# Kernel optimization log

Measured on AMD Instinct MI355X. Metric: run time of the kernel, lower is better.

Reference implementation:

```python
import jax, jax.numpy as jnp
import numpy as np

EMBED_DIM = 1024
NUM_HEADS = 16
HEAD_DIM = EMBED_DIM // NUM_HEADS


def setup_inputs() -> dict:
    key = jax.random.key(0)
    ks = jax.random.split(key, 10)
    s = 1.0 / np.sqrt(EMBED_DIM)
    inp = {
        "x1": jax.random.normal(ks[0], (4, 1024, EMBED_DIM), jnp.float32),
        "x2": jax.random.normal(ks[1], (4, 2048, EMBED_DIM), jnp.float32),
        "Wq": jax.random.normal(ks[2], (EMBED_DIM, EMBED_DIM), jnp.float32) * s,
        "bq": jnp.zeros((EMBED_DIM,), jnp.float32),
        "Wk": jax.random.normal(ks[3], (EMBED_DIM, EMBED_DIM), jnp.float32) * s,
        "bk": jnp.zeros((EMBED_DIM,), jnp.float32),
        "Wv": jax.random.normal(ks[4], (EMBED_DIM, EMBED_DIM), jnp.float32) * s,
        "bv": jnp.zeros((EMBED_DIM,), jnp.float32),
        "Wo": jax.random.normal(ks[5], (EMBED_DIM, EMBED_DIM), jnp.float32) * s,
        "bo": jnp.zeros((EMBED_DIM,), jnp.float32),
    }
    return inp


def reference(x1, x2, Wq, bq, Wk, bk, Wv, bv, Wo, bo):
    B, Sq, E = x1.shape
    Skv = x2.shape[1]
    H, D = NUM_HEADS, HEAD_DIM
    # linear projections (PyTorch Linear: x @ W.T + b)
    q = (x1 @ Wq.T + bq).reshape(B, Sq, H, D).transpose(0, 2, 1, 3)   # [B,H,Sq,D]
    k = (x2 @ Wk.T + bk).reshape(B, Skv, H, D).transpose(0, 2, 1, 3)  # [B,H,Skv,D]
    v = (x2 @ Wv.T + bv).reshape(B, Skv, H, D).transpose(0, 2, 1, 3)
    scores = jnp.einsum("bhqd,bhkd->bhqk", q, k) / jnp.sqrt(jnp.float32(D))
    attn = jax.nn.softmax(scores, axis=-1)
    out = jnp.einsum("bhqk,bhkd->bhqd", attn, v)
    out = out.transpose(0, 2, 1, 3).reshape(B, Sq, E)
    return out @ Wo.T + bo
```

## Files before the change

kernel.cpp:

```cpp
#include <hip/hip_runtime.h>

typedef __attribute__((ext_vector_type(8))) short short8;
typedef __attribute__((ext_vector_type(4))) short short4v;
typedef __attribute__((ext_vector_type(4))) float f32x4;
typedef _Float16 half8 __attribute__((ext_vector_type(8)));

#define ASYNC16(g, l) __builtin_amdgcn_global_load_lds( \
    (__attribute__((address_space(1))) void*)(g), \
    (__attribute__((address_space(3))) void*)(l), 16, 0, 0)

__device__ __forceinline__ short f2bf(float f) {
  union { float f; unsigned u; } v; v.f = f;
  unsigned r = v.u + 0x7fffu + ((v.u >> 16) & 1u);
  return (short)(r >> 16);
}

__device__ __forceinline__ short f2h(float f) {
  _Float16 h = (_Float16)f;
  return __builtin_bit_cast(short, h);
}

__device__ __forceinline__ unsigned pkh2(float a, float b) {
  return __builtin_bit_cast(unsigned, __builtin_amdgcn_cvt_pkrtz(a, b));
}

__device__ __forceinline__ f32x4 fzero4() {
  f32x4 z; z[0] = 0.f; z[1] = 0.f; z[2] = 0.f; z[3] = 0.f; return z;
}

__device__ __forceinline__ void wg_barrier() {
  asm volatile("s_waitcnt lgkmcnt(0)\n\ts_barrier" ::: "memory");
}

__device__ __forceinline__ void wait4_barrier() {
  asm volatile("s_waitcnt vmcnt(4)\n\ts_barrier" ::: "memory");
}
__device__ __forceinline__ void wait6_barrier() {
  asm volatile("s_waitcnt vmcnt(6)\n\ts_barrier" ::: "memory");
}
__device__ __forceinline__ void wait0_barrier() {
  asm volatile("s_waitcnt vmcnt(0)\n\ts_barrier" ::: "memory");
}

__global__ __launch_bounds__(256) void cvt_all(
    const float* __restrict__ x1, const float* __restrict__ x2,
    const float* __restrict__ wq, const float* __restrict__ wk,
    const float* __restrict__ wv, const float* __restrict__ wo,
    short* __restrict__ dst) {
  long e = ((long)blockIdx.x * 256 + threadIdx.x) * 4;
  const float* src; long loc;
  if (e < 4194304L)       { src = x1; loc = e; }
  else if (e < 12582912L) { src = x2; loc = e - 4194304L; }
  else if (e < 13631488L) { src = wq; loc = e - 12582912L; }
  else if (e < 14680064L) { src = wk; loc = e - 13631488L; }
  else if (e < 15728640L) { src = wv; loc = e - 14680064L; }
  else                    { src = wo; loc = e - 15728640L; }
  float4 v = *(const float4*)(src + loc);
  short4v o;
  o[0] = f2bf(v.x); o[1] = f2bf(v.y); o[2] = f2bf(v.z); o[3] = f2bf(v.w);
  *(short4v*)(dst + e) = o;
}

__global__ __launch_bounds__(256) void proj(
    const short* __restrict__ xb1, const short* __restrict__ xb2,
    const short* __restrict__ wqp, const short* __restrict__ wkp, const short* __restrict__ wvp,
    const float* __restrict__ bq, const float* __restrict__ bk, const float* __restrict__ bv,
    short* __restrict__ qb, short* __restrict__ kb, short* __restrict__ vb) {
  __shared__ short smem[16384];
  const int tid = threadIdx.x, w = tid >> 6, lane = tid & 63;
  const int quad = lane >> 4, col = lane & 15;
  const int waveM = (w >> 1) * 64, waveN = (w & 1) * 64;
  const int my = blockIdx.x, bn = blockIdx.y * 128;
  const short* A; const short* W; const float* bias; int mode, bm;
  if (my < 32)      { A = xb1; W = wqp; bias = bq; mode = 0; bm = my * 128; }
  else if (my < 96) { A = xb2; W = wkp; bias = bk; mode = 1; bm = (my - 32) * 128; }
  else              { A = xb2; W = wvp; bias = bv; mode = 2; bm = (my - 96) * 128; }

  f32x4 acc[4][4];
  for (int mi = 0; mi < 4; ++mi)
    for (int ni = 0; ni < 4; ++ni)
      acc[mi][ni] = fzero4();

  const int srow = w * 16 + (lane >> 2), scol = (lane & 3) * 8;
  const short* ga = A + (size_t)(bm + srow) * 1024 + scol;
  const short* gb = W + (size_t)(bn + srow) * 1024 + scol;

  auto stage = [&](int b, int kk) {
    short* lA = smem + b * 8192 + w * 512;
    short* lB = smem + b * 8192 + 4096 + w * 512;
    ASYNC16(ga + kk,         lA);
    ASYNC16(ga + kk + 65536, lA + 2048);
    ASYNC16(gb + kk,         lB);
    ASYNC16(gb + kk + 65536, lB + 2048);
  };
  auto compute = [&](int b) {
    const short* As_ = smem + b * 8192;
    const short* Bs_ = As_ + 4096;
    short8 af[4], bf[4];
    for (int mi = 0; mi < 4; ++mi)
      af[mi] = *(const short8*)(As_ + (waveM + mi * 16 + col) * 32 + quad * 8);
    for (int ni = 0; ni < 4; ++ni)
      bf[ni] = *(const short8*)(Bs_ + (waveN + ni * 16 + col) * 32 + quad * 8);
    for (int mi = 0; mi < 4; ++mi)
      for (int ni = 0; ni < 4; ++ni)
        acc[mi][ni] = __builtin_amdgcn_mfma_f32_16x16x32_bf16(af[mi], bf[ni], acc[mi][ni], 0, 0, 0);
  };

  stage(0, 0);
  stage(1, 32);
  for (int it = 0; it < 30; ++it) {
    wait4_barrier();
    compute(it & 1);
    wg_barrier();
    stage(it & 1, (it + 2) * 32);
  }
  wait4_barrier();
  compute(0);
  wait0_barrier();
  compute(1);

  for (int ni = 0; ni < 4; ++ni) {
    int nn = waveN + ni * 16 + col;
    float bvl = bias[bn + nn];
    for (int mi = 0; mi < 4; ++mi) {
      int m0 = waveM + mi * 16 + quad * 4;
      for (int r = 0; r < 4; ++r) {
        int m = m0 + r;
        float val = acc[mi][ni][r] + bvl;
        short sv;
        if (mode == 0)      sv = f2bf(val * 0.18033688011112042f);
        else if (mode == 1) sv = f2bf(val);
        else                sv = f2h(val);
        smem[m * 128 + (nn ^ ((m & 15) << 3))] = sv;
      }
    }
  }
  __syncthreads();
  if (mode < 2) {
    const int S = (mode == 0) ? 1024 : 2048;
    short* outp = (mode == 0) ? qb : kb;
    const int bb = bm / S, s0 = bm & (S - 1), h0 = bn >> 6;
    for (int it = 0; it < 8; ++it) {
      int f = (it * 256 + tid) * 8;
      int hh = f >> 13, rem = f & 8191, m = rem >> 6, d = rem & 63;
      int nn = hh * 64 + d;
      short8 val = *(const short8*)&smem[m * 128 + (nn ^ ((m & 15) << 3))];
      *(short8*)(outp + ((((size_t)(bb * 16 + h0 + hh)) * S + s0 + m) * 64 + d)) = val;
    }
  } else {
    const int bb = bm >> 11, s0 = bm & 2047, kt0 = s0 >> 6, h0 = bn >> 6;
    for (int it = 0; it < 8; ++it) {
      int f = (it * 256 + tid) * 8;
      int hh = f >> 13, rem = f & 8191, ktl = rem >> 12, r3 = rem & 4095;
      int d = r3 >> 6, kvp0 = r3 & 63;
      int nn = hh * 64 + d;
      short8 val;
      for (int j = 0; j < 8; ++j) {
        int kvp = kvp0 + j;
        int kv = ((kvp & 3) << 4) | (kvp >> 2);
        int m = ktl * 64 + kv;
        val[j] = smem[m * 128 + (nn ^ ((m & 15) << 3))];
      }
      *(short8*)(vb + ((((size_t)(bb * 16 + h0 + hh)) * 32 + (kt0 + ktl)) * 4096) + d * 64 + kvp0) = val;
    }
  }
}

__global__ __launch_bounds__(256) void out_gemm(
    const short* __restrict__ A, const short* __restrict__ W,
    const float* __restrict__ bias, float* __restrict__ out) {
  __shared__ short smem[24576];
  const int tid = threadIdx.x, w = tid >> 6, lane = tid & 63;
  const int quad = lane >> 4, col = lane & 15;
  const int waveM = (w >> 1) * 64, waveN = (w & 1) * 32;
  const int bn = blockIdx.x * 64, bm = blockIdx.y * 128;

  f32x4 acc[4][2];
  for (int mi = 0; mi < 4; ++mi)
    for (int ni = 0; ni < 2; ++ni)
      acc[mi][ni] = fzero4();

  const int arow = w * 16 + (lane >> 2), ac = (lane & 3) * 8;
  const short* ga = A + (size_t)(bm + arow) * 1024 + ac;
  const short* gb = W + (size_t)(bn + (tid >> 2)) * 1024 + (tid & 3) * 8;

  auto stage = [&](int b, int kk) {
    short* base = smem + b * 12288;
    short* lA0 = base + w * 512;
    short* lA1 = base + 4096 + w * 512;
    short* lB0 = base + 8192 + w * 512;
    short* lB1 = base + 10240 + w * 512;
    ASYNC16(ga + kk,              lA0);
    ASYNC16(ga + kk + 65536,      lA0 + 2048);
    ASYNC16(ga + kk + 32,         lA1);
    ASYNC16(ga + kk + 32 + 65536, lA1 + 2048);
    ASYNC16(gb + kk,              lB0);
    ASYNC16(gb + kk + 32,         lB1);
  };
  auto compute = [&](int b) {
    const short* base = smem + b * 12288;
    for (int kh = 0; kh < 2; ++kh) {
      const short* Ash = base + kh * 4096;
      const short* Bsh = base + 8192 + kh * 2048;
      short8 af[4], bf[2];
      for (int mi = 0; mi < 4; ++mi)
        af[mi] = *(const short8*)(Ash + (waveM + mi * 16 + col) * 32 + quad * 8);
      for (int ni = 0; ni < 2; ++ni)
        bf[ni] = *(const short8*)(Bsh + (waveN + ni * 16 + col) * 32 + quad * 8);
      for (int mi = 0; mi < 4; ++mi)
        for (int ni = 0; ni < 2; ++ni)
          acc[mi][ni] = __builtin_amdgcn_mfma_f32_16x16x32_bf16(af[mi], bf[ni], acc[mi][ni], 0, 0, 0);
    }
  };

  stage(0, 0);
  stage(1, 64);
  for (int it = 0; it < 14; ++it) {
    wait6_barrier();
    compute(it & 1);
    wg_barrier();
    stage(it & 1, (it + 2) * 64);
  }
  wait6_barrier();
  compute(0);
  wait0_barrier();
  compute(1);

  for (int ni = 0; ni < 2; ++ni) {
    int n = bn + waveN + ni * 16 + col;
    float bvl = bias[n];
    for (int mi = 0; mi < 4; ++mi) {
      int m0 = bm + waveM + mi * 16 + quad * 4;
      for (int r = 0; r < 4; ++r)
        out[(size_t)(m0 + r) * 1024 + n] = acc[mi][ni][r] + bvl;
    }
  }
}

__global__ __launch_bounds__(256, 2) void attn(
    const short* __restrict__ Q, const short* __restrict__ K,
    const short* __restrict__ V, short* __restrict__ O) {
  __shared__ short Ks[128 * 72];
  __shared__ short Vs[80 * 136];
  __shared__ short Ps[128 * 136];
  const int tid = threadIdx.x, w = tid >> 6, lane = tid & 63;
  const int quad = lane >> 4, col = lane & 15;
  const int bh = blockIdx.x, qt = blockIdx.y;
  const int b = bh >> 4, h = bh & 15;
  const int qbase = w * 32;

  const short* qp = Q + ((size_t)bh * 1024 + qt * 128) * 64;
  const short* kp = K + (size_t)bh * 131072;
  const short* vp = V + (size_t)bh * 131072;

  short8 aq[2][2];
  for (int mi = 0; mi < 2; ++mi) {
    const short* qr = qp + (qbase + mi * 16 + col) * 64 + quad * 8;
    aq[mi][0] = *(const short8*)qr;
    aq[mi][1] = *(const short8*)(qr + 32);
  }

  f32x4 oa[2][5];
  for (int mi = 0; mi < 2; ++mi)
    for (int ni = 0; ni < 5; ++ni)
      oa[mi][ni] = fzero4();

  for (int i = tid; i < 16 * 136; i += 256)
    Vs[64 * 136 + i] = (i < 136) ? (short)0x3C00 : (short)0;

  const int krow = lane + (w >> 1) * 64, kch = (w & 1) * 32;
  const int vd = lane, vch = w & 1, vkh = (w >> 1) * 32;

  short8 kpre[4], vpre[4];
  {
    const short* kg = kp + krow * 64 + kch;
    const short* vg = vp + vch * 4096 + vd * 64 + vkh;
    for (int i = 0; i < 4; ++i) kpre[i] = *(const short8*)(kg + i * 8);
    for (int i = 0; i < 4; ++i) vpre[i] = *(const short8*)(vg + i * 8);
  }

  for (int kt = 0; kt < 16; ++kt) {
    wg_barrier();
    for (int i = 0; i < 4; ++i)
      *(short8*)&Ks[krow * 72 + kch + i * 8] = kpre[i];
    for (int i = 0; i < 4; ++i)
      *(short8*)&Vs[vd * 136 + vch * 64 + vkh + i * 8] = vpre[i];
    {
      int ktn = (kt < 15) ? kt + 1 : kt;
      const short* kg = kp + ktn * 8192 + krow * 64 + kch;
      const short* vg = vp + (2 * ktn + vch) * 4096 + vd * 64 + vkh;
      for (int i = 0; i < 4; ++i) kpre[i] = *(const short8*)(kg + i * 8);
      for (int i = 0; i < 4; ++i) vpre[i] = *(const short8*)(vg + i * 8);
    }
    wg_barrier();

    f32x4 sf[2][8];
    for (int nk = 0; nk < 8; ++nk) {
      short8 bk0 = *(const short8*)&Ks[(nk * 16 + col) * 72 + quad * 8];
      short8 bk1 = *(const short8*)&Ks[(nk * 16 + col) * 72 + 32 + quad * 8];
      f32x4 z0 = fzero4(), z1 = fzero4();
      z0 = __builtin_amdgcn_mfma_f32_16x16x32_bf16(aq[0][0], bk0, z0, 0, 0, 0);
      z0 = __builtin_amdgcn_mfma_f32_16x16x32_bf16(aq[0][1], bk1, z0, 0, 0, 0);
      z1 = __builtin_amdgcn_mfma_f32_16x16x32_bf16(aq[1][0], bk0, z1, 0, 0, 0);
      z1 = __builtin_amdgcn_mfma_f32_16x16x32_bf16(aq[1][1], bk1, z1, 0, 0, 0);
      sf[0][nk] = z0;
      sf[1][nk] = z1;
    }

    for (int mi = 0; mi < 2; ++mi)
      for (int nk = 0; nk < 8; ++nk)
        for (int r = 0; r < 4; ++r)
          sf[mi][nk][r] = __builtin_amdgcn_exp2f(sf[mi][nk][r]);
    for (int mi = 0; mi < 2; ++mi)
      for (int r = 0; r < 4; ++r) {
        int row = qbase + mi * 16 + quad * 4 + r;
        uint2 d0, d1;
        d0.x = pkh2(sf[mi][0][r], sf[mi][1][r]);
        d0.y = pkh2(sf[mi][2][r], sf[mi][3][r]);
        d1.x = pkh2(sf[mi][4][r], sf[mi][5][r]);
        d1.y = pkh2(sf[mi][6][r], sf[mi][7][r]);
        *(uint2*)&Ps[row * 136 + col * 4]      = d0;
        *(uint2*)&Ps[row * 136 + 64 + col * 4] = d1;
      }

    for (int ks = 0; ks < 4; ++ks) {
      int koff = ks * 32 + quad * 8;
      half8 ap0 = *(const half8*)&Ps[(qbase + col) * 136 + koff];
      half8 ap1 = *(const half8*)&Ps[(qbase + 16 + col) * 136 + koff];
      for (int ni = 0; ni < 5; ++ni) {
        half8 bv = *(const half8*)&Vs[(ni * 16 + col) * 136 + koff];
        oa[0][ni] = __builtin_amdgcn_mfma_f32_16x16x32_f16(ap0, bv, oa[0][ni], 0, 0, 0);
        oa[1][ni] = __builtin_amdgcn_mfma_f32_16x16x32_f16(ap1, bv, oa[1][ni], 0, 0, 0);
      }
    }
  }

  float inv[2][4];
  for (int mi = 0; mi < 2; ++mi)
    for (int r = 0; r < 4; ++r) {
      float s = __shfl(oa[mi][4][r], lane & 48);
      inv[mi][r] = 1.f / s;
    }
  __syncthreads();
  for (int mi = 0; mi < 2; ++mi)
    for (int ni = 0; ni < 4; ++ni)
      for (int r = 0; r < 4; ++r)
        Ps[(qbase + mi * 16 + quad * 4 + r) * 64 + ni * 16 + col] = f2bf(oa[mi][ni][r] * inv[mi][r]);
  __syncthreads();
  for (int it = 0; it < 4; ++it) {
    int f = (it * 256 + tid) * 8;
    int q = f >> 6, d = f & 63;
    short8 val = *(const short8*)&Ps[q * 64 + d];
    *(short8*)(O + ((size_t)(b * 1024 + qt * 128 + q)) * 1024 + h * 64 + d) = val;
  }
}

extern "C" void kernel_launch(void* const* d_in, const int* in_sizes, int n_in,
                              void* d_out, int out_size, void* d_ws, size_t ws_size,
                              hipStream_t stream) {
  const float* x1 = (const float*)d_in[0];
  const float* x2 = (const float*)d_in[1];
  const float* Wq = (const float*)d_in[2];
  const float* bq = (const float*)d_in[3];
  const float* Wk = (const float*)d_in[4];
  const float* bk = (const float*)d_in[5];
  const float* Wv = (const float*)d_in[6];
  const float* bv = (const float*)d_in[7];
  const float* Wo = (const float*)d_in[8];
  const float* bo = (const float*)d_in[9];

  char* ws = (char*)d_ws;
  short* xb1 = (short*)(ws + 0);
  short* xb2 = (short*)(ws + 8388608);
  short* wqb = (short*)(ws + 25165824);
  short* wkb = (short*)(ws + 27262976);
  short* wvb = (short*)(ws + 29360128);
  short* wob = (short*)(ws + 31457280);
  short* qb  = (short*)(ws + 33554432);
  short* kb  = (short*)(ws + 41943040);
  short* vb  = (short*)(ws + 58720256);
  short* ob  = (short*)(ws + 75497472);

  cvt_all<<<16384, 256, 0, stream>>>(x1, x2, Wq, Wk, Wv, Wo, (short*)ws);
  proj<<<dim3(160, 8), 256, 0, stream>>>(xb1, xb2, wqb, wkb, wvb, bq, bk, bv, qb, kb, vb);
  attn<<<dim3(64, 8), 256, 0, stream>>>(qb, kb, vb, ob);
  out_gemm<<<dim3(16, 32), 256, 0, stream>>>(ob, wob, bo, (float*)d_out);
}
```

Baseline: 233.9 us.

## Replace QKV GEMM async double buffering with single-buffer 64-wide K steps; register ones row

The QKV projection GEMM drops its two-stage async pipeline with vmcnt waits. Each iteration now loads a 64-wide K chunk into two LDS halves, waits at a full __syncthreads, then computes both halves, so the loop has fewer iterations and fewer barriers but no overlap of loads with MFMA. In attention, the row-sum ones block is no longer stored in LDS Vs. It becomes a register constant fed to a separate MFMA, which shrinks shared memory and drops one LDS read per k-step.

```diff
diff --git a/kernel.cpp b/kernel.cpp
--- a/kernel.cpp
+++ b/kernel.cpp
@@ -32,9 +32,6 @@
   asm volatile("s_waitcnt lgkmcnt(0)\n\ts_barrier" ::: "memory");
 }
 
-__device__ __forceinline__ void wait4_barrier() {
-  asm volatile("s_waitcnt vmcnt(4)\n\ts_barrier" ::: "memory");
-}
 __device__ __forceinline__ void wait6_barrier() {
   asm volatile("s_waitcnt vmcnt(6)\n\ts_barrier" ::: "memory");
 }
@@ -84,41 +81,37 @@
   const int srow = w * 16 + (lane >> 2), scol = (lane & 3) * 8;
   const short* ga = A + (size_t)(bm + srow) * 1024 + scol;
   const short* gb = W + (size_t)(bn + srow) * 1024 + scol;
-
-  auto stage = [&](int b, int kk) {
-    short* lA = smem + b * 8192 + w * 512;
-    short* lB = smem + b * 8192 + 4096 + w * 512;
-    ASYNC16(ga + kk,         lA);
-    ASYNC16(ga + kk + 65536, lA + 2048);
-    ASYNC16(gb + kk,         lB);
-    ASYNC16(gb + kk + 65536, lB + 2048);
-  };
-  auto compute = [&](int b) {
-    const short* As_ = smem + b * 8192;
-    const short* Bs_ = As_ + 4096;
-    short8 af[4], bf[4];
-    for (int mi = 0; mi < 4; ++mi)
-      af[mi] = *(const short8*)(As_ + (waveM + mi * 16 + col) * 32 + quad * 8);
-    for (int ni = 0; ni < 4; ++ni)
-      bf[ni] = *(const short8*)(Bs_ + (waveN + ni * 16 + col) * 32 + quad * 8);
-    for (int mi = 0; mi < 4; ++mi)
+  short* lA0 = smem + w * 512;
+  short* lA1 = smem + 4096 + w * 512;
+  short* lB0 = smem + 8192 + w * 512;
+  short* lB1 = smem + 12288 + w * 512;
+
+  for (int kk = 0; kk < 1024; kk += 64) {
+    __syncthreads();
+    ASYNC16(ga + kk,              lA0);
+    ASYNC16(ga + kk + 65536,      lA0 + 2048);
+    ASYNC16(ga + kk + 32,         lA1);
+    ASYNC16(ga + kk + 32 + 65536, lA1 + 2048);
+    ASYNC16(gb + kk,              lB0);
+    ASYNC16(gb + kk + 65536,      lB0 + 2048);
+    ASYNC16(gb + kk + 32,         lB1);
+    ASYNC16(gb + kk + 32 + 65536, lB1 + 2048);
+    __syncthreads();
+    for (int kh = 0; kh < 2; ++kh) {
+      const short* As_ = smem + kh * 4096;
+      const short* Bs_ = smem + 8192 + kh * 4096;
+      short8 af[4], bf[4];
+      for (int mi = 0; mi < 4; ++mi)
+        af[mi] = *(const short8*)(As_ + (waveM + mi * 16 + col) * 32 + quad * 8);
       for (int ni = 0; ni < 4; ++ni)
-        acc[mi][ni] = __builtin_amdgcn_mfma_f32_16x16x32_bf16(af[mi], bf[ni], acc[mi][ni], 0, 0, 0);
-  };
-
-  stage(0, 0);
-  stage(1, 32);
-  for (int it = 0; it < 30; ++it) {
-    wait4_barrier();
-    compute(it & 1);
-    wg_barrier();
-    stage(it & 1, (it + 2) * 32);
-  }
-  wait4_barrier();
-  compute(0);
-  wait0_barrier();
-  compute(1);
-
+        bf[ni] = *(const short8*)(Bs_ + (waveN + ni * 16 + col) * 32 + quad * 8);
+      for (int mi = 0; mi < 4; ++mi)
+        for (int ni = 0; ni < 4; ++ni)
+          acc[mi][ni] = __builtin_amdgcn_mfma_f32_16x16x32_bf16(af[mi], bf[ni], acc[mi][ni], 0, 0, 0);
+    }
+  }
+
+  __syncthreads();
   for (int ni = 0; ni < 4; ++ni) {
     int nn = waveN + ni * 16 + col;
     float bvl = bias[bn + nn];
@@ -241,7 +234,7 @@
     const short* __restrict__ Q, const short* __restrict__ K,
     const short* __restrict__ V, short* __restrict__ O) {
   __shared__ short Ks[128 * 72];
-  __shared__ short Vs[80 * 136];
+  __shared__ short Vs[64 * 136];
   __shared__ short Ps[128 * 136];
   const int tid = threadIdx.x, w = tid >> 6, lane = tid & 63;
   const int quad = lane >> 4, col = lane & 15;
@@ -265,8 +258,8 @@
     for (int ni = 0; ni < 5; ++ni)
       oa[mi][ni] = fzero4();
 
-  for (int i = tid; i < 16 * 136; i += 256)
-    Vs[64 * 136 + i] = (i < 136) ? (short)0x3C00 : (short)0;
+  half8 bones;
+  for (int j = 0; j < 8; ++j) bones[j] = (col == 0) ? (_Float16)1.0f : (_Float16)0.0f;
 
   const int krow = lane + (w >> 1) * 64, kch = (w & 1) * 32;
   const int vd = lane, vch = w & 1, vkh = (w >> 1) * 32;
@@ -327,11 +320,13 @@
       int koff = ks * 32 + quad * 8;
       half8 ap0 = *(const half8*)&Ps[(qbase + col) * 136 + koff];
       half8 ap1 = *(const half8*)&Ps[(qbase + 16 + col) * 136 + koff];
-      for (int ni = 0; ni < 5; ++ni) {
+      for (int ni = 0; ni < 4; ++ni) {
         half8 bv = *(const half8*)&Vs[(ni * 16 + col) * 136 + koff];
         oa[0][ni] = __builtin_amdgcn_mfma_f32_16x16x32_f16(ap0, bv, oa[0][ni], 0, 0, 0);
         oa[1][ni] = __builtin_amdgcn_mfma_f32_16x16x32_f16(ap1, bv, oa[1][ni], 0, 0, 0);
       }
+      oa[0][4] = __builtin_amdgcn_mfma_f32_16x16x32_f16(ap0, bones, oa[0][4], 0, 0, 0);
+      oa[1][4] = __builtin_amdgcn_mfma_f32_16x16x32_f16(ap1, bones, oa[1][4], 0, 0, 0);
     }
   }
 
```

After: 244.8 us. 1.05x slower.
